# Optimization experiments

Hardware: AMD Instinct MI355X
Metric: run time of the kernel (lower is better)

The kernel has to match this reference:

```python
import jax, jax.numpy as jnp
import numpy as np
import math

C = 256
K = 64
STAGE_NUM = 3
UNFOLD_SIZES = (1, 3, 5)


def _l2norm(t, axis):
    return t / (1e-6 + jnp.linalg.norm(t, axis=axis, keepdims=True))


def setup_inputs() -> dict:
    key = jax.random.key(0)
    k0, k1, k2 = jax.random.split(key, 3)
    b, h, w = 4, 64, 64
    x = jax.random.normal(k0, (b, C, h, w), dtype=jnp.float32)
    mu0 = jax.random.normal(k1, (1, C, K), dtype=jnp.float32) * math.sqrt(2.0 / K)
    mu0 = _l2norm(mu0, axis=1)  # matches buffer init: normal_(0, sqrt(2/k)) then l2norm over c
    w_scalar = jnp.array(1.0, dtype=jnp.float32)
    # convcat: Conv2d(3c, c, 1); init std = sqrt(2 / (1*1*out_channels)) = sqrt(2/c)
    w_cat = jax.random.normal(k2, (C, 3 * C), dtype=jnp.float32) * math.sqrt(2.0 / C)
    b_cat = jnp.zeros((C,), dtype=jnp.float32)
    return {"x": x, "mu0": mu0, "w": w_scalar, "w_cat": w_cat, "b_cat": b_cat}


def _mwi_forward(x, mu0, w, w_cat, b_cat):
    b, c, h, wd = x.shape
    k = mu0.shape[2]
    mu = jnp.broadcast_to(mu0, (b, c, k))
    feats = []
    for s in UNFOLD_SIZES:
        p = (s - 1) // 2
        xp = jnp.pad(x, ((0, 0), (0, 0), (p, p), (p, p)))
        # im2col: (b, c, s*s, h, w), kernel positions row-major -> matches torch F.unfold then view(b,c,-1)
        patches = jnp.stack([xp[:, :, i:i + h, j:j + wd] for i in range(s) for j in range(s)], axis=2)
        ux = patches.reshape(b, c, s * s * h * wd)  # (b, c, N)
        z = None
        for _ in range(STAGE_NUM):  # EM iterations (no_grad in original)
            z = jax.nn.softmax(jnp.einsum('bcn,bck->bnk', ux, mu), axis=2)  # E-step
            z_ = z / (1e-6 + z.sum(axis=1, keepdims=True))
            mu = _l2norm(jnp.einsum('bcn,bnk->bck', ux, z_), axis=1)  # M-step
        mu = jax.lax.stop_gradient(mu)
        z = jax.lax.stop_gradient(z)
        zf = jnp.einsum('bck,bnk->bcn', mu, z)  # reconstruction (b, c, N)
        zf = zf.reshape(b, c, s, s, h, wd)
        # col2im (F.fold): overlap-add of kernel positions
        out = jnp.zeros((b, c, h + 2 * p, wd + 2 * p), dtype=x.dtype)
        for i in range(s):
            for j in range(s):
                out = out.at[:, :, i:i + h, j:j + wd].add(zf[:, :, i, j])
        feats.append(out[:, :, p:p + h, p:p + wd])
    cat = jnp.concatenate(feats, axis=1)  # (b, 3c, h, w)
    u = jnp.einsum('bihw,oi->bohw', cat, w_cat) + b_cat[None, :, None, None]
    out = jax.nn.relu(u * w + x)
    return out, mu


def reference(x, mu0, w, w_cat, b_cat):
    return _mwi_forward(x, mu0, w, w_cat, b_cat)
```

## Files before the change

### kernel.cpp

```cpp
#include <hip/hip_runtime.h>

typedef float f32x4 __attribute__((ext_vector_type(4)));
typedef short bf16x8 __attribute__((ext_vector_type(8)));
typedef unsigned short u16;
typedef u16 u16x8 __attribute__((ext_vector_type(8)));
typedef unsigned int u32;

#define B 4
#define C 256
#define K 64
#define NN 4096
#define W3C 768
#define CP 264
#define SP 72

__device__ __forceinline__ u16 bf_hi(float f) {
    unsigned u = __float_as_uint(f);
    u += 0x7FFFu + ((u >> 16) & 1u);
    return (u16)(u >> 16);
}
__device__ __forceinline__ float bf_f(u16 s) { return __uint_as_float(((unsigned)s) << 16); }

__global__ void k_prep(const float* __restrict__ x, const float* __restrict__ mu0,
                       const float* __restrict__ w_cat,
                       u16* __restrict__ xch, u16* __restrict__ xcl,
                       u16* __restrict__ wch, u16* __restrict__ wcl,
                       u16* __restrict__ muth, u16* __restrict__ mutl) {
    int blk = blockIdx.x, tid = threadIdx.x;
    if (blk < 2048) {
        int i = blk * 256 + tid;
        const float4* s4 = (const float4*)(x + (size_t)i * 8);
        float4 a = s4[0], bq = s4[1];
        float v[8] = {a.x, a.y, a.z, a.w, bq.x, bq.y, bq.z, bq.w};
        u16x8 hv, lv;
        #pragma unroll
        for (int j = 0; j < 8; j++) { u16 hh = bf_hi(v[j]); hv[j] = hh; lv[j] = bf_hi(v[j] - bf_f(hh)); }
        *(u16x8*)(xch + (size_t)i * 8) = hv;
        *(u16x8*)(xcl + (size_t)i * 8) = lv;
    } else if (blk < 2144) {
        int i = (blk - 2048) * 256 + tid;
        const float4* s4 = (const float4*)(w_cat + (size_t)i * 8);
        float4 a = s4[0], bq = s4[1];
        float v[8] = {a.x, a.y, a.z, a.w, bq.x, bq.y, bq.z, bq.w};
        u16x8 hv, lv;
        #pragma unroll
        for (int j = 0; j < 8; j++) { u16 hh = bf_hi(v[j]); hv[j] = hh; lv[j] = bf_hi(v[j] - bf_f(hh)); }
        *(u16x8*)(wch + (size_t)i * 8) = hv;
        *(u16x8*)(wcl + (size_t)i * 8) = lv;
    } else {
        int g = (blk - 2144) * 256 + tid;
        int kq = (g >> 8) & 63, cq = g & 255;
        float v = mu0[cq * K + kq];
        u16 hh = bf_hi(v);
        muth[g] = hh;
        mutl[g] = bf_hi(v - bf_f(hh));
    }
}

__global__ void k_prept(const float* __restrict__ x, u16* __restrict__ th,
                        u16* __restrict__ tl) {
    __shared__ float tile[32][33];
    int b = blockIdx.z, c0 = blockIdx.y * 32, n0 = blockIdx.x * 32;
    int tx = threadIdx.x, ty = threadIdx.y;
    #pragma unroll
    for (int j = 0; j < 4; j++)
        tile[ty + j * 8][tx] = x[((size_t)(b * C + c0 + ty + j * 8)) * NN + n0 + tx];
    __syncthreads();
    #pragma unroll
    for (int j = 0; j < 4; j++) {
        int n = n0 + ty + j * 8;
        float v = tile[tx][ty + j * 8];
        u16 hh = bf_hi(v);
        size_t o = ((size_t)(b * NN + n)) * C + c0 + tx;
        th[o] = hh;
        tl[o] = bf_hi(v - bf_f(hh));
    }
}

__global__ __launch_bounds__(256) void k_em(
        const u16* __restrict__ xth, const u16* __restrict__ xtl,
        const u16* __restrict__ xch, const u16* __restrict__ xcl,
        const u16* __restrict__ muth, const u16* __restrict__ mutl,
        float* __restrict__ tpart, float* __restrict__ dpart,
        u16* __restrict__ sig_out, int pv, int write_sig)
{
    extern __shared__ char smem[];
    u16* smh = (u16*)smem;
    u16* sml = smh + 64 * CP;
    u16* sTh = sml + 64 * CP;
    u16* sTl = sTh + 64 * SP;
    float* redf = (float*)(sTl + 64 * SP);

    const int ch = blockIdx.x, b = blockIdx.y, tid = threadIdx.x;
    const int n0 = ch * 64;

    {
        size_t mbase = ((size_t)(b * K)) * C;
        for (int t = tid; t < 2048; t += 256) {
            int r = t >> 5, cof = (t & 31) * 8;
            *(u16x8*)&smh[r * CP + cof] = *(const u16x8*)&muth[mbase + (size_t)r * C + cof];
            *(u16x8*)&sml[r * CP + cof] = *(const u16x8*)&mutl[mbase + (size_t)r * C + cof];
        }
    }
    __syncthreads();

    const int wid = tid >> 6, l = tid & 63, lg = l >> 4, lr = l & 15;
    f32x4 z4 = {0.f, 0.f, 0.f, 0.f};

    f32x4 acc[4] = {z4, z4, z4, z4};
    {
        const u16* xrh = xth + ((size_t)(b * NN + n0 + wid * 16 + lr)) * C;
        const u16* xrl = xtl + ((size_t)(b * NN + n0 + wid * 16 + lr)) * C;
        for (int cc = 0; cc < 8; cc++) {
            int co = cc * 32 + lg * 8;
            bf16x8 Ah = *(const bf16x8*)&xrh[co];
            bf16x8 Al = *(const bf16x8*)&xrl[co];
            #pragma unroll
            for (int kt = 0; kt < 4; kt++) {
                bf16x8 Bh = *(bf16x8*)&smh[(kt * 16 + lr) * CP + co];
                bf16x8 Bl = *(bf16x8*)&sml[(kt * 16 + lr) * CP + co];
                acc[kt] = __builtin_amdgcn_mfma_f32_16x16x32_bf16(Ah, Bh, acc[kt], 0, 0, 0);
                acc[kt] = __builtin_amdgcn_mfma_f32_16x16x32_bf16(Al, Bh, acc[kt], 0, 0, 0);
                acc[kt] = __builtin_amdgcn_mfma_f32_16x16x32_bf16(Ah, Bl, acc[kt], 0, 0, 0);
            }
        }
    }

    float swv[4][4];
    float psum[4] = {0.f, 0.f, 0.f, 0.f};
    #pragma unroll
    for (int jj = 0; jj < 4; jj++) {
        int n = n0 + wid * 16 + lg * 4 + jj;
        float v0 = acc[0][jj], v1 = acc[1][jj], v2 = acc[2][jj], v3 = acc[3][jj];
        float m = fmaxf(fmaxf(v0, v1), fmaxf(v2, v3));
        #pragma unroll
        for (int off = 1; off <= 8; off <<= 1) m = fmaxf(m, __shfl_xor(m, off));
        float e0 = __expf(v0 - m), e1 = __expf(v1 - m), e2 = __expf(v2 - m), e3 = __expf(v3 - m);
        float ss = e0 + e1 + e2 + e3;
        #pragma unroll
        for (int off = 1; off <= 8; off <<= 1) ss += __shfl_xor(ss, off);
        int y = n >> 6, xx = n & 63;
        float cnt = (float)((min(pv, y) + min(pv, 63 - y) + 1) * (min(pv, xx) + min(pv, 63 - xx) + 1));
        float sc = cnt / ss;
        swv[jj][0] = e0 * sc; swv[jj][1] = e1 * sc; swv[jj][2] = e2 * sc; swv[jj][3] = e3 * sc;
        #pragma unroll
        for (int kt = 0; kt < 4; kt++) {
            psum[kt] += swv[jj][kt];
            if (write_sig)
                sig_out[((size_t)(b * NN + n)) * K + kt * 16 + lr] = bf_hi(swv[jj][kt]);
        }
    }
    #pragma unroll
    for (int kt = 0; kt < 4; kt++) {
        #pragma unroll
        for (int jp = 0; jp < 2; jp++) {
            float va = swv[2 * jp][kt], vb = swv[2 * jp + 1][kt];
            u16 ha = bf_hi(va), hb = bf_hi(vb);
            u16 la = bf_hi(va - bf_f(ha)), lb = bf_hi(vb - bf_f(hb));
            int col = wid * 16 + lg * 4 + 2 * jp;
            *(u32*)&sTh[(kt * 16 + lr) * SP + col] = (u32)ha | ((u32)hb << 16);
            *(u32*)&sTl[(kt * 16 + lr) * SP + col] = (u32)la | ((u32)lb << 16);
        }
        redf[(kt * 16 + lr) * 17 + wid * 4 + lg] = psum[kt];
    }
    __syncthreads();
    if (tid < 64) {
        float sd = 0.f;
        #pragma unroll
        for (int g2 = 0; g2 < 16; g2++) sd += redf[tid * 17 + g2];
        dpart[((size_t)(b * 64 + ch)) * K + tid] = sd;
    }

    f32x4 macc[16];
    #pragma unroll
    for (int ci = 0; ci < 16; ci++) macc[ci] = z4;
    #pragma unroll
    for (int nn2 = 0; nn2 < 2; nn2++) {
        int no = nn2 * 32 + lg * 8;
        bf16x8 Ah = *(bf16x8*)&sTh[(wid * 16 + lr) * SP + no];
        bf16x8 Al = *(bf16x8*)&sTl[(wid * 16 + lr) * SP + no];
        #pragma unroll
        for (int ci = 0; ci < 16; ci++) {
            size_t go = ((size_t)(b * C + ci * 16 + lr)) * NN + n0 + no;
            bf16x8 Bh = *(const bf16x8*)&xch[go];
            bf16x8 Bl = *(const bf16x8*)&xcl[go];
            macc[ci] = __builtin_amdgcn_mfma_f32_16x16x32_bf16(Ah, Bh, macc[ci], 0, 0, 0);
            macc[ci] = __builtin_amdgcn_mfma_f32_16x16x32_bf16(Al, Bh, macc[ci], 0, 0, 0);
            macc[ci] = __builtin_amdgcn_mfma_f32_16x16x32_bf16(Ah, Bl, macc[ci], 0, 0, 0);
        }
    }
    #pragma unroll
    for (int ci = 0; ci < 16; ci++)
        #pragma unroll
        for (int jj = 0; jj < 4; jj++)
            tpart[((size_t)((b * 64 + ch) * K + wid * 16 + lg * 4 + jj)) * C + ci * 16 + lr]
                = macc[ci][jj];
}

__global__ __launch_bounds__(256) void k_norm(
        const float* __restrict__ tpart, const float* __restrict__ dpart,
        u16* __restrict__ muth, u16* __restrict__ mutl,
        float* __restrict__ out_mu, float dconst) {
    __shared__ float red[256];
    __shared__ float dsh;
    int k = blockIdx.x, b = blockIdx.y, tid = threadIdx.x;
    float dv = 0.f;
    if (tid < 64) dv = dpart[((size_t)(b * 64 + tid)) * K + k];
    #pragma unroll
    for (int off = 1; off <= 32; off <<= 1) dv += __shfl_xor(dv, off);
    if (tid == 0) dsh = dv;
    float tt = 0.f;
    #pragma unroll 8
    for (int chn = 0; chn < 64; chn++)
        tt += tpart[((size_t)((b * 64 + chn) * K + k)) * C + tid];
    red[tid] = tt * tt;
    __syncthreads();
    for (int st = 128; st > 0; st >>= 1) {
        if (tid < st) red[tid] += red[tid + st];
        __syncthreads();
    }
    float d = dconst + dsh;
    float inv = 1.f / (1e-6f * d + sqrtf(red[0]));
    float v = tt * inv;
    u16 hh = bf_hi(v);
    size_t o = ((size_t)(b * K + k)) * C + tid;
    muth[o] = hh;
    mutl[o] = bf_hi(v - bf_f(hh));
    out_mu[((size_t)(b * C + tid)) * K + k] = v;
}

__global__ __launch_bounds__(256) void k_pmat(
        const u16* __restrict__ wch, const u16* __restrict__ wcl,
        const u16* __restrict__ mh_g, const u16* __restrict__ ml_g,
        u16* __restrict__ Pb, int s) {
    int ob = blockIdx.x, b = blockIdx.y;
    int tid = threadIdx.x, w = tid >> 6, l = tid & 63, lg = l >> 4, lr = l & 15;
    f32x4 z4 = {0.f, 0.f, 0.f, 0.f};
    f32x4 acc[4] = {z4, z4, z4, z4};
    int orow = ob * 64 + w * 16 + lr;
    const u16* wbh = wch + (size_t)orow * W3C + s * C;
    const u16* wbl = wcl + (size_t)orow * W3C + s * C;
    for (int cc = 0; cc < 8; cc++) {
        int co = cc * 32 + lg * 8;
        bf16x8 Ah = *(const bf16x8*)&wbh[co];
        bf16x8 Al = *(const bf16x8*)&wbl[co];
        #pragma unroll
        for (int kt = 0; kt < 4; kt++) {
            bf16x8 Bh = *(const bf16x8*)&mh_g[((size_t)(b * K + kt * 16 + lr)) * C + co];
            bf16x8 Bl = *(const bf16x8*)&ml_g[((size_t)(b * K + kt * 16 + lr)) * C + co];
            acc[kt] = __builtin_amdgcn_mfma_f32_16x16x32_bf16(Ah, Bh, acc[kt], 0, 0, 0);
            acc[kt] = __builtin_amdgcn_mfma_f32_16x16x32_bf16(Al, Bh, acc[kt], 0, 0, 0);
            acc[kt] = __builtin_amdgcn_mfma_f32_16x16x32_bf16(Ah, Bl, acc[kt], 0, 0, 0);
        }
    }
    #pragma unroll
    for (int kt = 0; kt < 4; kt++)
        #pragma unroll
        for (int jj = 0; jj < 4; jj++) {
            int o = ob * 64 + w * 16 + lg * 4 + jj;
            Pb[((size_t)((s * B + b) * C + o)) * K + kt * 16 + lr] = bf_hi(acc[kt][jj]);
        }
}

__global__ __launch_bounds__(256) void k_final(
        const u16* __restrict__ sh_g, const u16* __restrict__ Pb,
        const float* __restrict__ x, const float* __restrict__ b_cat,
        const float* __restrict__ wscal, float* __restrict__ out) {
    __shared__ u16 ssig[64 * 72];
    __shared__ u16 sP[64 * 72];
    __shared__ float tbuf[64 * 68];
    int nt = blockIdx.x, ot = blockIdx.y, b = blockIdx.z;
    int n0 = nt * 64, o0 = ot * 64;
    int tid = threadIdx.x, w = tid >> 6, l = tid & 63, lg = l >> 4, lr = l & 15;
    f32x4 z4 = {0.f, 0.f, 0.f, 0.f};
    f32x4 acc[4] = {z4, z4, z4, z4};
    for (int s = 0; s < 3; s++) {
        __syncthreads();
        for (int t = tid; t < 512; t += 256) {
            int r = t >> 3, kc = (t & 7) * 8;
            *(u16x8*)&ssig[r * 72 + kc] =
                *(const u16x8*)&sh_g[(size_t)s * ((size_t)B * NN * K) + ((size_t)(b * NN + n0 + r)) * K + kc];
            *(u16x8*)&sP[r * 72 + kc] =
                *(const u16x8*)&Pb[((size_t)((s * B + b) * C + o0 + r)) * K + kc];
        }
        __syncthreads();
        #pragma unroll
        for (int kk = 0; kk < 2; kk++) {
            int ko = kk * 32 + lg * 8;
            bf16x8 A = *(bf16x8*)&ssig[(w * 16 + lr) * 72 + ko];
            #pragma unroll
            for (int oi = 0; oi < 4; oi++) {
                bf16x8 Bv = *(bf16x8*)&sP[(oi * 16 + lr) * 72 + ko];
                acc[oi] = __builtin_amdgcn_mfma_f32_16x16x32_bf16(A, Bv, acc[oi], 0, 0, 0);
            }
        }
    }
    __syncthreads();
    #pragma unroll
    for (int oi = 0; oi < 4; oi++)
        #pragma unroll
        for (int jj = 0; jj < 4; jj++)
            tbuf[(oi * 16 + lr) * 68 + (w * 16 + lg * 4 + jj)] = acc[oi][jj];
    __syncthreads();
    float wv = wscal[0];
    for (int t = tid; t < 1024; t += 256) {
        int ol = t >> 4, ck = (t & 15) * 4;
        int o = o0 + ol;
        float bc = b_cat[o];
        float4 u4 = *(float4*)&tbuf[ol * 68 + ck];
        size_t base = ((size_t)(b * C + o)) * NN + n0 + ck;
        float4 xv = *(const float4*)&x[base];
        float4 r;
        r.x = fmaxf((u4.x + bc) * wv + xv.x, 0.f);
        r.y = fmaxf((u4.y + bc) * wv + xv.y, 0.f);
        r.z = fmaxf((u4.z + bc) * wv + xv.z, 0.f);
        r.w = fmaxf((u4.w + bc) * wv + xv.w, 0.f);
        *(float4*)&out[base] = r;
    }
}

extern "C" void kernel_launch(void* const* d_in, const int* in_sizes, int n_in,
                              void* d_out, int out_size, void* d_ws, size_t ws_size,
                              hipStream_t stream) {
    const float* x     = (const float*)d_in[0];
    const float* mu0   = (const float*)d_in[1];
    const float* wsc   = (const float*)d_in[2];
    const float* w_cat = (const float*)d_in[3];
    const float* b_cat = (const float*)d_in[4];
    float* out = (float*)d_out;
    char* wsb = (char*)d_ws;

    const size_t SZ_X2   = (size_t)B * C * NN * 2;
    const size_t SZ_MUT  = (size_t)B * K * C * 2;
    const size_t SZ_SIGH = (size_t)3 * B * NN * K * 2;
    const size_t SZ_TP   = (size_t)B * 64 * K * C * 4;
    const size_t SZ_DP   = (size_t)B * 64 * K * 4;
    const size_t SZ_PB   = (size_t)3 * B * C * K * 2;
    const size_t SZ_WC   = (size_t)C * W3C * 2;

    size_t off = 0;
    u16*   xch  = (u16*)(wsb + off); off += SZ_X2;
    u16*   xcl  = (u16*)(wsb + off); off += SZ_X2;
    u16*   xth  = (u16*)(wsb + off); off += SZ_X2;
    u16*   xtl  = (u16*)(wsb + off); off += SZ_X2;
    u16*   muth = (u16*)(wsb + off); off += SZ_MUT;
    u16*   mutl = (u16*)(wsb + off); off += SZ_MUT;
    u16*   sigh = (u16*)(wsb + off); off += SZ_SIGH;
    float* tpart= (float*)(wsb + off); off += SZ_TP;
    float* dpart= (float*)(wsb + off); off += SZ_DP;
    u16*   Pb   = (u16*)(wsb + off); off += SZ_PB;
    u16*   wch  = (u16*)(wsb + off); off += SZ_WC;
    u16*   wcl  = (u16*)(wsb + off); off += SZ_WC;
    float* out_mu = out + (size_t)B * C * NN;

    const int EM_LDS = 2 * 64 * CP * 2 + 2 * 64 * SP * 2 + 1088 * 4;
    hipFuncSetAttribute((const void*)k_em, hipFuncAttributeMaxDynamicSharedMemorySize, EM_LDS);

    k_prep<<<2400, 256, 0, stream>>>(x, mu0, w_cat, xch, xcl, wch, wcl, muth, mutl);
    k_prept<<<dim3(128, 8, B), dim3(32, 8), 0, stream>>>(x, xth, xtl);

    const int   pvals[3]   = {0, 1, 2};
    const float dconsts[3] = {1e-6f, 1e-6f + 11.9375f, 1e-6f + 59.4375f};

    for (int s = 0; s < 3; s++) {
        u16* shs = sigh + (size_t)s * ((size_t)B * NN * K);
        for (int it = 0; it < 3; it++) {
            k_em<<<dim3(64, B), 256, EM_LDS, stream>>>(xth, xtl, xch, xcl, muth, mutl,
                                                       tpart, dpart, shs, pvals[s],
                                                       (it == 2) ? 1 : 0);
            k_norm<<<dim3(K, B), 256, 0, stream>>>(tpart, dpart, muth, mutl,
                                                   out_mu, dconsts[s]);
        }
        k_pmat<<<dim3(4, B), 256, 0, stream>>>(wch, wcl, muth, mutl, Pb, s);
    }
    k_final<<<dim3(64, 4, B), 256, 0, stream>>>(sigh, Pb, x, b_cat, wsc, out);
}
```

Measured before the change: 298.7 us.

## Split EM kernel across 8 waves, fuse pmat into norm and transpose into prep

The EM kernel now runs 512 threads: the E-step logits are split over two channel halves and reduced through LDS, and the M-step is repartitioned so each wave owns 32 channels and preloads its x tiles into registers before the barrier. The separate k_pmat launch is folded into k_norm as a scalar dot product per output channel, and the transpose kernel is merged into k_prep. The out_mu store now happens only on the last iteration. These changes cut launch count and raise per-block parallelism, but add an LDS round trip, idle half-waves during softmax, and a slower scalar matmul for the P matrix.

```diff
diff --git a/kernel.cpp b/kernel.cpp
--- a/kernel.cpp
+++ b/kernel.cpp
@@ -13,6 +13,7 @@
 #define W3C 768
 #define CP 264
 #define SP 72
+#define LGP 68
 
 __device__ __forceinline__ u16 bf_hi(float f) {
     unsigned u = __float_as_uint(f);
@@ -25,7 +26,9 @@
                        const float* __restrict__ w_cat,
                        u16* __restrict__ xch, u16* __restrict__ xcl,
                        u16* __restrict__ wch, u16* __restrict__ wcl,
-                       u16* __restrict__ muth, u16* __restrict__ mutl) {
+                       u16* __restrict__ muth, u16* __restrict__ mutl,
+                       u16* __restrict__ xth, u16* __restrict__ xtl) {
+    __shared__ float tile[32][33];
     int blk = blockIdx.x, tid = threadIdx.x;
     if (blk < 2048) {
         int i = blk * 256 + tid;
@@ -47,37 +50,35 @@
         for (int j = 0; j < 8; j++) { u16 hh = bf_hi(v[j]); hv[j] = hh; lv[j] = bf_hi(v[j] - bf_f(hh)); }
         *(u16x8*)(wch + (size_t)i * 8) = hv;
         *(u16x8*)(wcl + (size_t)i * 8) = lv;
-    } else {
+    } else if (blk < 2400) {
         int g = (blk - 2144) * 256 + tid;
         int kq = (g >> 8) & 63, cq = g & 255;
         float v = mu0[cq * K + kq];
         u16 hh = bf_hi(v);
         muth[g] = hh;
         mutl[g] = bf_hi(v - bf_f(hh));
-    }
-}
-
-__global__ void k_prept(const float* __restrict__ x, u16* __restrict__ th,
-                        u16* __restrict__ tl) {
-    __shared__ float tile[32][33];
-    int b = blockIdx.z, c0 = blockIdx.y * 32, n0 = blockIdx.x * 32;
-    int tx = threadIdx.x, ty = threadIdx.y;
-    #pragma unroll
-    for (int j = 0; j < 4; j++)
-        tile[ty + j * 8][tx] = x[((size_t)(b * C + c0 + ty + j * 8)) * NN + n0 + tx];
-    __syncthreads();
-    #pragma unroll
-    for (int j = 0; j < 4; j++) {
-        int n = n0 + ty + j * 8;
-        float v = tile[tx][ty + j * 8];
-        u16 hh = bf_hi(v);
-        size_t o = ((size_t)(b * NN + n)) * C + c0 + tx;
-        th[o] = hh;
-        tl[o] = bf_hi(v - bf_f(hh));
-    }
-}
-
-__global__ __launch_bounds__(256) void k_em(
+    } else {
+        int t = blk - 2400;
+        int b2 = t >> 10, rem = t & 1023;
+        int c0 = (rem >> 7) << 5, m0 = (rem & 127) << 5;
+        int tx = tid & 31, ty = tid >> 5;
+        #pragma unroll
+        for (int j = 0; j < 4; j++)
+            tile[ty + j * 8][tx] = x[((size_t)(b2 * C + c0 + ty + j * 8)) * NN + m0 + tx];
+        __syncthreads();
+        #pragma unroll
+        for (int j = 0; j < 4; j++) {
+            int n = m0 + ty + j * 8;
+            float v = tile[tx][ty + j * 8];
+            u16 hh = bf_hi(v);
+            size_t o = ((size_t)(b2 * NN + n)) * C + c0 + tx;
+            xth[o] = hh;
+            xtl[o] = bf_hi(v - bf_f(hh));
+        }
+    }
+}
+
+__global__ __launch_bounds__(512) void k_em(
         const u16* __restrict__ xth, const u16* __restrict__ xtl,
         const u16* __restrict__ xch, const u16* __restrict__ xcl,
         const u16* __restrict__ muth, const u16* __restrict__ mutl,
@@ -87,81 +88,112 @@
     extern __shared__ char smem[];
     u16* smh = (u16*)smem;
     u16* sml = smh + 64 * CP;
-    u16* sTh = sml + 64 * CP;
+    float* slog = (float*)(sml + 64 * CP);
+    u16* sTh = (u16*)(slog + 64 * LGP);
     u16* sTl = sTh + 64 * SP;
     float* redf = (float*)(sTl + 64 * SP);
 
     const int ch = blockIdx.x, b = blockIdx.y, tid = threadIdx.x;
     const int n0 = ch * 64;
+    const int w = tid >> 6, l = tid & 63, lg = l >> 4, lr = l & 15;
+    const int chalf = (w >> 2) * 128;
+    f32x4 z4 = {0.f, 0.f, 0.f, 0.f};
 
     {
-        size_t mbase = ((size_t)(b * K)) * C;
-        for (int t = tid; t < 2048; t += 256) {
+        size_t mbase = (size_t)(b * K) * C;
+        #pragma unroll
+        for (int t = tid; t < 2048; t += 512) {
             int r = t >> 5, cof = (t & 31) * 8;
             *(u16x8*)&smh[r * CP + cof] = *(const u16x8*)&muth[mbase + (size_t)r * C + cof];
             *(u16x8*)&sml[r * CP + cof] = *(const u16x8*)&mutl[mbase + (size_t)r * C + cof];
         }
     }
-    __syncthreads();
-
-    const int wid = tid >> 6, l = tid & 63, lg = l >> 4, lr = l & 15;
-    f32x4 z4 = {0.f, 0.f, 0.f, 0.f};
+    bf16x8 eAh[4], eAl[4];
+    {
+        const u16* xrh = xth + ((size_t)(b * NN + n0 + (w & 3) * 16 + lr)) * C + chalf;
+        const u16* xrl = xtl + ((size_t)(b * NN + n0 + (w & 3) * 16 + lr)) * C + chalf;
+        #pragma unroll
+        for (int cc = 0; cc < 4; cc++) {
+            eAh[cc] = *(const bf16x8*)&xrh[cc * 32 + lg * 8];
+            eAl[cc] = *(const bf16x8*)&xrl[cc * 32 + lg * 8];
+        }
+    }
+    bf16x8 mBh[4], mBl[4];
+    #pragma unroll
+    for (int nn2 = 0; nn2 < 2; nn2++)
+        #pragma unroll
+        for (int cio = 0; cio < 2; cio++) {
+            int c = (w * 2 + cio) * 16 + lr;
+            size_t go = ((size_t)(b * C + c)) * NN + n0 + nn2 * 32 + lg * 8;
+            mBh[nn2 * 2 + cio] = *(const bf16x8*)&xch[go];
+            mBl[nn2 * 2 + cio] = *(const bf16x8*)&xcl[go];
+        }
+    __syncthreads();
 
     f32x4 acc[4] = {z4, z4, z4, z4};
-    {
-        const u16* xrh = xth + ((size_t)(b * NN + n0 + wid * 16 + lr)) * C;
-        const u16* xrl = xtl + ((size_t)(b * NN + n0 + wid * 16 + lr)) * C;
-        for (int cc = 0; cc < 8; cc++) {
-            int co = cc * 32 + lg * 8;
-            bf16x8 Ah = *(const bf16x8*)&xrh[co];
-            bf16x8 Al = *(const bf16x8*)&xrl[co];
+    #pragma unroll
+    for (int cc = 0; cc < 4; cc++) {
+        int co = chalf + cc * 32 + lg * 8;
+        #pragma unroll
+        for (int kt = 0; kt < 4; kt++) {
+            bf16x8 Bh = *(bf16x8*)&smh[(kt * 16 + lr) * CP + co];
+            bf16x8 Bl = *(bf16x8*)&sml[(kt * 16 + lr) * CP + co];
+            acc[kt] = __builtin_amdgcn_mfma_f32_16x16x32_bf16(eAh[cc], Bh, acc[kt], 0, 0, 0);
+            acc[kt] = __builtin_amdgcn_mfma_f32_16x16x32_bf16(eAl[cc], Bh, acc[kt], 0, 0, 0);
+            acc[kt] = __builtin_amdgcn_mfma_f32_16x16x32_bf16(eAh[cc], Bl, acc[kt], 0, 0, 0);
+        }
+    }
+    if (w < 4) {
+        #pragma unroll
+        for (int kt = 0; kt < 4; kt++)
+            #pragma unroll
+            for (int jj = 0; jj < 4; jj++)
+                slog[((w & 3) * 16 + lg * 4 + jj) * LGP + kt * 16 + lr] = acc[kt][jj];
+    }
+    __syncthreads();
+
+    if (w >= 4) {
+        float swv[4][4];
+        float psum[4] = {0.f, 0.f, 0.f, 0.f};
+        #pragma unroll
+        for (int jj = 0; jj < 4; jj++) {
+            int rloc = (w & 3) * 16 + lg * 4 + jj;
+            int n = n0 + rloc;
+            float v0 = acc[0][jj] + slog[rloc * LGP + 0 * 16 + lr];
+            float v1 = acc[1][jj] + slog[rloc * LGP + 1 * 16 + lr];
+            float v2 = acc[2][jj] + slog[rloc * LGP + 2 * 16 + lr];
+            float v3 = acc[3][jj] + slog[rloc * LGP + 3 * 16 + lr];
+            float m = fmaxf(fmaxf(v0, v1), fmaxf(v2, v3));
+            #pragma unroll
+            for (int off = 1; off <= 8; off <<= 1) m = fmaxf(m, __shfl_xor(m, off));
+            float e0 = __expf(v0 - m), e1 = __expf(v1 - m), e2 = __expf(v2 - m), e3 = __expf(v3 - m);
+            float ss = e0 + e1 + e2 + e3;
+            #pragma unroll
+            for (int off = 1; off <= 8; off <<= 1) ss += __shfl_xor(ss, off);
+            int y = n >> 6, xx = n & 63;
+            float cntw = (float)((min(pv, y) + min(pv, 63 - y) + 1) * (min(pv, xx) + min(pv, 63 - xx) + 1));
+            float sc = cntw / ss;
+            swv[jj][0] = e0 * sc; swv[jj][1] = e1 * sc; swv[jj][2] = e2 * sc; swv[jj][3] = e3 * sc;
             #pragma unroll
             for (int kt = 0; kt < 4; kt++) {
-                bf16x8 Bh = *(bf16x8*)&smh[(kt * 16 + lr) * CP + co];
-                bf16x8 Bl = *(bf16x8*)&sml[(kt * 16 + lr) * CP + co];
-                acc[kt] = __builtin_amdgcn_mfma_f32_16x16x32_bf16(Ah, Bh, acc[kt], 0, 0, 0);
-                acc[kt] = __builtin_amdgcn_mfma_f32_16x16x32_bf16(Al, Bh, acc[kt], 0, 0, 0);
-                acc[kt] = __builtin_amdgcn_mfma_f32_16x16x32_bf16(Ah, Bl, acc[kt], 0, 0, 0);
-            }
-        }
-    }
-
-    float swv[4][4];
-    float psum[4] = {0.f, 0.f, 0.f, 0.f};
-    #pragma unroll
-    for (int jj = 0; jj < 4; jj++) {
-        int n = n0 + wid * 16 + lg * 4 + jj;
-        float v0 = acc[0][jj], v1 = acc[1][jj], v2 = acc[2][jj], v3 = acc[3][jj];
-        float m = fmaxf(fmaxf(v0, v1), fmaxf(v2, v3));
-        #pragma unroll
-        for (int off = 1; off <= 8; off <<= 1) m = fmaxf(m, __shfl_xor(m, off));
-        float e0 = __expf(v0 - m), e1 = __expf(v1 - m), e2 = __expf(v2 - m), e3 = __expf(v3 - m);
-        float ss = e0 + e1 + e2 + e3;
-        #pragma unroll
-        for (int off = 1; off <= 8; off <<= 1) ss += __shfl_xor(ss, off);
-        int y = n >> 6, xx = n & 63;
-        float cnt = (float)((min(pv, y) + min(pv, 63 - y) + 1) * (min(pv, xx) + min(pv, 63 - xx) + 1));
-        float sc = cnt / ss;
-        swv[jj][0] = e0 * sc; swv[jj][1] = e1 * sc; swv[jj][2] = e2 * sc; swv[jj][3] = e3 * sc;
+                psum[kt] += swv[jj][kt];
+                if (write_sig)
+                    sig_out[((size_t)(b * NN + n)) * K + kt * 16 + lr] = bf_hi(swv[jj][kt]);
+            }
+        }
         #pragma unroll
         for (int kt = 0; kt < 4; kt++) {
-            psum[kt] += swv[jj][kt];
-            if (write_sig)
-                sig_out[((size_t)(b * NN + n)) * K + kt * 16 + lr] = bf_hi(swv[jj][kt]);
-        }
-    }
-    #pragma unroll
-    for (int kt = 0; kt < 4; kt++) {
-        #pragma unroll
-        for (int jp = 0; jp < 2; jp++) {
-            float va = swv[2 * jp][kt], vb = swv[2 * jp + 1][kt];
-            u16 ha = bf_hi(va), hb = bf_hi(vb);
-            u16 la = bf_hi(va - bf_f(ha)), lb = bf_hi(vb - bf_f(hb));
-            int col = wid * 16 + lg * 4 + 2 * jp;
-            *(u32*)&sTh[(kt * 16 + lr) * SP + col] = (u32)ha | ((u32)hb << 16);
-            *(u32*)&sTl[(kt * 16 + lr) * SP + col] = (u32)la | ((u32)lb << 16);
-        }
-        redf[(kt * 16 + lr) * 17 + wid * 4 + lg] = psum[kt];
+            #pragma unroll
+            for (int jp = 0; jp < 2; jp++) {
+                float va = swv[2 * jp][kt], vb = swv[2 * jp + 1][kt];
+                u16 ha = bf_hi(va), hb = bf_hi(vb);
+                u16 la = bf_hi(va - bf_f(ha)), lb = bf_hi(vb - bf_f(hb));
+                int col = (w & 3) * 16 + lg * 4 + 2 * jp;
+                *(u32*)&sTh[(kt * 16 + lr) * SP + col] = (u32)ha | ((u32)hb << 16);
+                *(u32*)&sTl[(kt * 16 + lr) * SP + col] = (u32)la | ((u32)lb << 16);
+            }
+            redf[(kt * 16 + lr) * 17 + (w & 3) * 4 + lg] = psum[kt];
+        }
     }
     __syncthreads();
     if (tid < 64) {
@@ -171,37 +203,47 @@
         dpart[((size_t)(b * 64 + ch)) * K + tid] = sd;
     }
 
-    f32x4 macc[16];
-    #pragma unroll
-    for (int ci = 0; ci < 16; ci++) macc[ci] = z4;
+    f32x4 macc[8];
+    #pragma unroll
+    for (int t2 = 0; t2 < 8; t2++) macc[t2] = z4;
     #pragma unroll
     for (int nn2 = 0; nn2 < 2; nn2++) {
         int no = nn2 * 32 + lg * 8;
-        bf16x8 Ah = *(bf16x8*)&sTh[(wid * 16 + lr) * SP + no];
-        bf16x8 Al = *(bf16x8*)&sTl[(wid * 16 + lr) * SP + no];
-        #pragma unroll
-        for (int ci = 0; ci < 16; ci++) {
-            size_t go = ((size_t)(b * C + ci * 16 + lr)) * NN + n0 + no;
-            bf16x8 Bh = *(const bf16x8*)&xch[go];
-            bf16x8 Bl = *(const bf16x8*)&xcl[go];
-            macc[ci] = __builtin_amdgcn_mfma_f32_16x16x32_bf16(Ah, Bh, macc[ci], 0, 0, 0);
-            macc[ci] = __builtin_amdgcn_mfma_f32_16x16x32_bf16(Al, Bh, macc[ci], 0, 0, 0);
-            macc[ci] = __builtin_amdgcn_mfma_f32_16x16x32_bf16(Ah, Bl, macc[ci], 0, 0, 0);
-        }
-    }
-    #pragma unroll
-    for (int ci = 0; ci < 16; ci++)
-        #pragma unroll
-        for (int jj = 0; jj < 4; jj++)
-            tpart[((size_t)((b * 64 + ch) * K + wid * 16 + lg * 4 + jj)) * C + ci * 16 + lr]
-                = macc[ci][jj];
+        bf16x8 Ah[4], Al[4];
+        #pragma unroll
+        for (int kt2 = 0; kt2 < 4; kt2++) {
+            Ah[kt2] = *(bf16x8*)&sTh[(kt2 * 16 + lr) * SP + no];
+            Al[kt2] = *(bf16x8*)&sTl[(kt2 * 16 + lr) * SP + no];
+        }
+        #pragma unroll
+        for (int cio = 0; cio < 2; cio++) {
+            #pragma unroll
+            for (int kt2 = 0; kt2 < 4; kt2++) {
+                macc[kt2 * 2 + cio] = __builtin_amdgcn_mfma_f32_16x16x32_bf16(Ah[kt2], mBh[nn2 * 2 + cio], macc[kt2 * 2 + cio], 0, 0, 0);
+                macc[kt2 * 2 + cio] = __builtin_amdgcn_mfma_f32_16x16x32_bf16(Al[kt2], mBh[nn2 * 2 + cio], macc[kt2 * 2 + cio], 0, 0, 0);
+                macc[kt2 * 2 + cio] = __builtin_amdgcn_mfma_f32_16x16x32_bf16(Ah[kt2], mBl[nn2 * 2 + cio], macc[kt2 * 2 + cio], 0, 0, 0);
+            }
+        }
+    }
+    #pragma unroll
+    for (int kt2 = 0; kt2 < 4; kt2++)
+        #pragma unroll
+        for (int cio = 0; cio < 2; cio++)
+            #pragma unroll
+            for (int jj = 0; jj < 4; jj++) {
+                int kk = kt2 * 16 + lg * 4 + jj;
+                int c = (w * 2 + cio) * 16 + lr;
+                tpart[((size_t)((b * 64 + ch) * K + kk)) * C + c] = macc[kt2 * 2 + cio][jj];
+            }
 }
 
 __global__ __launch_bounds__(256) void k_norm(
         const float* __restrict__ tpart, const float* __restrict__ dpart,
         u16* __restrict__ muth, u16* __restrict__ mutl,
-        float* __restrict__ out_mu, float dconst) {
+        u16* __restrict__ Pb, const u16* __restrict__ wch, const u16* __restrict__ wcl,
+        float* __restrict__ out_mu, float dconst, int s_pm, int last) {
     __shared__ float red[256];
+    __shared__ float murow[256];
     __shared__ float dsh;
     int k = blockIdx.x, b = blockIdx.y, tid = threadIdx.x;
     float dv = 0.f;
@@ -222,44 +264,27 @@
     float d = dconst + dsh;
     float inv = 1.f / (1e-6f * d + sqrtf(red[0]));
     float v = tt * inv;
+    murow[tid] = v;
     u16 hh = bf_hi(v);
     size_t o = ((size_t)(b * K + k)) * C + tid;
     muth[o] = hh;
     mutl[o] = bf_hi(v - bf_f(hh));
-    out_mu[((size_t)(b * C + tid)) * K + k] = v;
-}
-
-__global__ __launch_bounds__(256) void k_pmat(
-        const u16* __restrict__ wch, const u16* __restrict__ wcl,
-        const u16* __restrict__ mh_g, const u16* __restrict__ ml_g,
-        u16* __restrict__ Pb, int s) {
-    int ob = blockIdx.x, b = blockIdx.y;
-    int tid = threadIdx.x, w = tid >> 6, l = tid & 63, lg = l >> 4, lr = l & 15;
-    f32x4 z4 = {0.f, 0.f, 0.f, 0.f};
-    f32x4 acc[4] = {z4, z4, z4, z4};
-    int orow = ob * 64 + w * 16 + lr;
-    const u16* wbh = wch + (size_t)orow * W3C + s * C;
-    const u16* wbl = wcl + (size_t)orow * W3C + s * C;
-    for (int cc = 0; cc < 8; cc++) {
-        int co = cc * 32 + lg * 8;
-        bf16x8 Ah = *(const bf16x8*)&wbh[co];
-        bf16x8 Al = *(const bf16x8*)&wbl[co];
-        #pragma unroll
-        for (int kt = 0; kt < 4; kt++) {
-            bf16x8 Bh = *(const bf16x8*)&mh_g[((size_t)(b * K + kt * 16 + lr)) * C + co];
-            bf16x8 Bl = *(const bf16x8*)&ml_g[((size_t)(b * K + kt * 16 + lr)) * C + co];
-            acc[kt] = __builtin_amdgcn_mfma_f32_16x16x32_bf16(Ah, Bh, acc[kt], 0, 0, 0);
-            acc[kt] = __builtin_amdgcn_mfma_f32_16x16x32_bf16(Al, Bh, acc[kt], 0, 0, 0);
-            acc[kt] = __builtin_amdgcn_mfma_f32_16x16x32_bf16(Ah, Bl, acc[kt], 0, 0, 0);
-        }
-    }
-    #pragma unroll
-    for (int kt = 0; kt < 4; kt++)
-        #pragma unroll
-        for (int jj = 0; jj < 4; jj++) {
-            int o = ob * 64 + w * 16 + lg * 4 + jj;
-            Pb[((size_t)((s * B + b) * C + o)) * K + kt * 16 + lr] = bf_hi(acc[kt][jj]);
-        }
+    if (last) out_mu[((size_t)(b * C + tid)) * K + k] = v;
+    if (s_pm >= 0) {
+        __syncthreads();
+        const u16* wh = wch + (size_t)tid * W3C + s_pm * C;
+        const u16* wl = wcl + (size_t)tid * W3C + s_pm * C;
+        float accp = 0.f;
+        #pragma unroll 4
+        for (int c8 = 0; c8 < 32; c8++) {
+            u16x8 hv = *(const u16x8*)&wh[c8 * 8];
+            u16x8 lv = *(const u16x8*)&wl[c8 * 8];
+            #pragma unroll
+            for (int j = 0; j < 8; j++)
+                accp += (bf_f(hv[j]) + bf_f(lv[j])) * murow[c8 * 8 + j];
+        }
+        Pb[((size_t)((s_pm * B + b) * C + tid)) * K + k] = bf_hi(accp);
+    }
 }
 
 __global__ __launch_bounds__(256) void k_final(
@@ -353,25 +378,21 @@
     u16*   wcl  = (u16*)(wsb + off); off += SZ_WC;
     float* out_mu = out + (size_t)B * C * NN;
 
-    const int EM_LDS = 2 * 64 * CP * 2 + 2 * 64 * SP * 2 + 1088 * 4;
+    const int EM_LDS = 2 * 64 * CP * 2 + 64 * LGP * 4 + 2 * 64 * SP * 2 + 1152 * 4;
     hipFuncSetAttribute((const void*)k_em, hipFuncAttributeMaxDynamicSharedMemorySize, EM_LDS);
 
-    k_prep<<<2400, 256, 0, stream>>>(x, mu0, w_cat, xch, xcl, wch, wcl, muth, mutl);
-    k_prept<<<dim3(128, 8, B), dim3(32, 8), 0, stream>>>(x, xth, xtl);
-
-    const int   pvals[3]   = {0, 1, 2};
+    k_prep<<<6496, 256, 0, stream>>>(x, mu0, w_cat, xch, xcl, wch, wcl, muth, mutl, xth, xtl);
+
     const float dconsts[3] = {1e-6f, 1e-6f + 11.9375f, 1e-6f + 59.4375f};
 
-    for (int s = 0; s < 3; s++) {
+    for (int i = 0; i < 9; i++) {
+        int s = i / 3;
         u16* shs = sigh + (size_t)s * ((size_t)B * NN * K);
-        for (int it = 0; it < 3; it++) {
-            k_em<<<dim3(64, B), 256, EM_LDS, stream>>>(xth, xtl, xch, xcl, muth, mutl,
-                                                       tpart, dpart, shs, pvals[s],
-                                                       (it == 2) ? 1 : 0);
-            k_norm<<<dim3(K, B), 256, 0, stream>>>(tpart, dpart, muth, mutl,
-                                                   out_mu, dconsts[s]);
-        }
-        k_pmat<<<dim3(4, B), 256, 0, stream>>>(wch, wcl, muth, mutl, Pb, s);
+        k_em<<<dim3(64, B), 512, EM_LDS, stream>>>(
+            xth, xtl, xch, xcl, muth, mutl, tpart, dpart, shs, s, (i % 3 == 2) ? 1 : 0);
+        k_norm<<<dim3(K, B), 256, 0, stream>>>(
+            tpart, dpart, muth, mutl, Pb, wch, wcl, out_mu,
+            dconsts[s], (i % 3 == 2) ? s : -1, (i == 8) ? 1 : 0);
     }
     k_final<<<dim3(64, 4, B), 256, 0, stream>>>(sigh, Pb, x, b_cat, wsc, out);
 }
```

After: 259.6 us (median of 2 runs). -13.1%, faster.
